# Optimization experiments

Hardware: AMD Instinct MI355X
Metric: run time of the kernel (lower is better)

Reference implementation:

```python
import jax, jax.numpy as jnp
import numpy as np

N = 100_000   # nodes
E = 800_000   # edges
G = 2048      # graphs in batch
IN, H = 74, 256
M1, M2 = 1024, 512


def setup_inputs() -> dict:
    key = jax.random.key(0)
    ks = jax.random.split(key, 16)
    h = jax.random.normal(ks[0], (N, IN), dtype=jnp.float32)
    src = jax.random.randint(ks[1], (E,), 0, N, dtype=jnp.int32)
    dst = jax.random.randint(ks[2], (E,), 0, N, dtype=jnp.int32)
    gid = jnp.sort(jax.random.randint(ks[3], (N,), 0, G, dtype=jnp.int32))
    s = lambda d: 1.0 / np.sqrt(d)
    W_in = jax.random.normal(ks[4], (IN, H), dtype=jnp.float32) * s(IN)
    b_in = jnp.zeros((H,), jnp.float32)
    W_gcr = jax.random.normal(ks[5], (10, H, H), dtype=jnp.float32) * s(H)  # 5 GCR x 2 convs
    b_gcr = jnp.zeros((10, H), jnp.float32)
    W1 = jax.random.normal(ks[6], (H, M1), dtype=jnp.float32) * s(H)
    b1 = jnp.zeros((M1,), jnp.float32)
    W2 = jax.random.normal(ks[7], (M1, M2), dtype=jnp.float32) * s(M1)
    b2 = jnp.zeros((M2,), jnp.float32)
    W3 = jax.random.normal(ks[8], (M2, 1), dtype=jnp.float32) * s(M2)
    b3 = jnp.zeros((1,), jnp.float32)
    return dict(h=h, src=src, dst=dst, gid=gid, W_in=W_in, b_in=b_in,
                W_gcr=W_gcr, b_gcr=b_gcr, W1=W1, b1=b1, W2=W2, b2=b2, W3=W3, b3=b3)


def _graph_conv(x, W, b, src, dst, out_norm, in_norm):
    # DGL GraphConv, norm='both': D_out^{-1/2} -> SpMM(copy_u,sum) -> D_in^{-1/2} -> linear
    x = x * out_norm[:, None]
    m = jax.ops.segment_sum(x[src], dst, num_segments=N)
    m = m * in_norm[:, None]
    return m @ W + b


def reference(h, src, dst, gid, W_in, b_in, W_gcr, b_gcr, W1, b1, W2, b2, W3, b3):
    ones_e = jnp.ones((E,), jnp.float32)
    out_deg = jax.ops.segment_sum(ones_e, src, num_segments=N)
    in_deg = jax.ops.segment_sum(ones_e, dst, num_segments=N)
    out_norm = jax.lax.rsqrt(jnp.maximum(out_deg, 1.0))
    in_norm = jax.lax.rsqrt(jnp.maximum(in_deg, 1.0))

    x = _graph_conv(h, W_in, b_in, src, dst, out_norm, in_norm)  # no activation here
    for i in range(5):  # GCR: gcn1 -> relu -> gcn2 -> relu
        y = _graph_conv(x, W_gcr[2 * i], b_gcr[2 * i], src, dst, out_norm, in_norm)
        y = _graph_conv(jax.nn.relu(y), W_gcr[2 * i + 1], b_gcr[2 * i + 1], src, dst, out_norm, in_norm)
        x = jax.nn.relu(y)  # res_connection=0 -> plain replace

    # dgl.mean_nodes per graph
    sums = jax.ops.segment_sum(x, gid, num_segments=G)
    cnts = jax.ops.segment_sum(jnp.ones((N,), jnp.float32), gid, num_segments=G)
    node_mean = sums / jnp.maximum(cnts, 1.0)[:, None]

    z = jax.nn.leaky_relu(node_mean @ W1 + b1)
    z = jax.nn.leaky_relu(z @ W2 + b2)
    out = (z @ W3 + b3).squeeze(-1)  # [G]
    return out
```

## Files before the change

### kernel.cpp

```cpp
#include <hip/hip_runtime.h>
#include <hip/hip_bf16.h>

#define NN 100000
#define NE 800000
#define NG 2048
#define DIN 74
#define KPAD 96
#define DH 256
#define DM1 1024
#define DM2 512

typedef __attribute__((ext_vector_type(8))) short short8;
typedef __attribute__((ext_vector_type(4))) float f32x4;

__device__ inline ushort f2bf(float f) {
  unsigned u = __float_as_uint(f);
  return (ushort)((u + 0x7fffu + ((u >> 16) & 1u)) >> 16);
}
__device__ inline float bf2f(ushort h) { return __uint_as_float(((unsigned)h) << 16); }

__device__ inline void gll16(const ushort* g, ushort* l) {
  __builtin_amdgcn_global_load_lds((const __attribute__((address_space(1))) void*)g,
                                   (__attribute__((address_space(3))) void*)l, 16, 0, 0);
}

__global__ void k_deg(const int* __restrict__ src, const int* __restrict__ dst,
                      int* __restrict__ outd, int* __restrict__ ind) {
  int e = blockIdx.x * blockDim.x + threadIdx.x;
  if (e < NE) {
    atomicAdd(&outd[src[e]], 1);
    atomicAdd(&ind[dst[e]], 1);
  }
}

__global__ void k_norm(const int* __restrict__ outd, const int* __restrict__ ind,
                       float* __restrict__ onorm, float* __restrict__ inorm) {
  int i = blockIdx.x * blockDim.x + threadIdx.x;
  if (i < NN) {
    onorm[i] = rsqrtf(fmaxf((float)outd[i], 1.f));
    inorm[i] = rsqrtf(fmaxf((float)ind[i], 1.f));
  }
}

__global__ void k_scan_block(const int* __restrict__ deg, int* __restrict__ incl,
                             int* __restrict__ bsum, int n) {
  __shared__ int s[1024];
  int t = threadIdx.x;
  int i = blockIdx.x * 1024 + t;
  int v = (i < n) ? deg[i] : 0;
  s[t] = v;
  __syncthreads();
  for (int off = 1; off < 1024; off <<= 1) {
    int x = (t >= off) ? s[t - off] : 0;
    __syncthreads();
    s[t] += x;
    __syncthreads();
  }
  if (i < n) incl[i] = s[t];
  if (t == 1023) bsum[blockIdx.x] = s[1023];
}

__global__ void k_scan_sums(int* bsum, int nb) {
  int lane = threadIdx.x & 63;
  int i0 = 2 * lane, i1 = 2 * lane + 1;
  int v0 = (i0 < nb) ? bsum[i0] : 0;
  int v1 = (i1 < nb) ? bsum[i1] : 0;
  int s = v0 + v1;
  for (int off = 1; off < 64; off <<= 1) {
    int t = __shfl_up(s, off);
    if (lane >= off) s += t;
  }
  int excl = s - (v0 + v1);
  if (i0 < nb) bsum[i0] = excl;
  if (i1 < nb) bsum[i1] = excl + v0;
}

__global__ void k_scan_add(const int* __restrict__ incl, const int* __restrict__ bsum,
                           const int* __restrict__ deg,
                           int* __restrict__ offs, int* __restrict__ cursor, int n) {
  int i = blockIdx.x * blockDim.x + threadIdx.x;
  if (i < n) {
    int v = incl[i] + bsum[i >> 10];
    offs[i + 1] = v;
    cursor[i] = v - deg[i];
    if (i == 0) offs[0] = 0;
  }
}

__global__ void k_scatter(const int* __restrict__ src, const int* __restrict__ dst,
                          int* __restrict__ cursor, int* __restrict__ ssrc) {
  int e = blockIdx.x * blockDim.x + threadIdx.x;
  if (e < NE) {
    int pos = atomicAdd(&cursor[dst[e]], 1);
    ssrc[pos] = src[e];
  }
}

__global__ void k_convw(const float* __restrict__ W_in, const float* __restrict__ W_gcr,
                        const float* __restrict__ W1, const float* __restrict__ W2,
                        ushort* __restrict__ Wt0h, ushort* __restrict__ Wt0l,
                        ushort* __restrict__ Wtgh, ushort* __restrict__ Wtgl,
                        ushort* __restrict__ Wt1h, ushort* __restrict__ Wt1l,
                        ushort* __restrict__ Wt2h, ushort* __restrict__ Wt2l) {
  int idx = blockIdx.x * blockDim.x + threadIdx.x;
  const int n0 = 256 * KPAD;
  const int n1 = n0 + 10 * 65536;
  const int n2 = n1 + DM1 * DH;
  const int n3 = n2 + DM2 * DM1;
  float v;
  ushort *dh, *dl;
  int o;
  if (idx < n0) {
    int n = idx / KPAD, k = idx - n * KPAD;
    v = (k < DIN) ? W_in[k * DH + n] : 0.f;
    dh = Wt0h; dl = Wt0l; o = idx;
  } else if (idx < n1) {
    int j = idx - n0;
    int l = j >> 16, r = j & 65535;
    int n = r >> 8, k = r & 255;
    v = W_gcr[l * 65536 + k * 256 + n];
    dh = Wtgh; dl = Wtgl; o = l * 65536 + n * 256 + k;
  } else if (idx < n2) {
    int j = idx - n1;
    int n = j >> 8, k = j & 255;
    v = W1[k * DM1 + n];
    dh = Wt1h; dl = Wt1l; o = n * 256 + k;
  } else if (idx < n3) {
    int j = idx - n2;
    int n = j >> 10, k = j & 1023;
    v = W2[k * DM2 + n];
    dh = Wt2h; dl = Wt2l; o = n * 1024 + k;
  } else {
    return;
  }
  ushort hv = f2bf(v);
  dh[o] = hv;
  dl[o] = f2bf(v - bf2f(hv));
}

__global__ void k_spmm74(const float* __restrict__ h, const int* __restrict__ offs,
                         const int* __restrict__ ssrc, const float* __restrict__ onorm,
                         const float* __restrict__ inorm,
                         ushort* __restrict__ Ahi, ushort* __restrict__ Alo) {
  int row = blockIdx.x * 4 + (threadIdx.x >> 6);
  if (row >= NN) return;
  int lane = threadIdx.x & 63;
  int beg = offs[row], end = offs[row + 1];
  float a0 = 0.f, a1 = 0.f;
  for (int e = beg; e < end; ++e) {
    int s = ssrc[e];
    float w = onorm[s];
    const float* hr = h + (size_t)s * DIN;
    a0 += w * hr[lane];
    if (lane < DIN - 64) a1 += w * hr[64 + lane];
  }
  float win = inorm[row];
  ushort* ph = Ahi + (size_t)row * KPAD;
  ushort* pl = Alo + (size_t)row * KPAD;
  float v0 = a0 * win;
  ushort h0 = f2bf(v0);
  ph[lane] = h0;
  pl[lane] = f2bf(v0 - bf2f(h0));
  if (lane < DIN - 64) {
    float v1 = a1 * win;
    ushort h1 = f2bf(v1);
    ph[64 + lane] = h1;
    pl[64 + lane] = f2bf(v1 - bf2f(h1));
  } else if (lane < KPAD - 64) {
    ph[64 + lane] = 0;
    pl[64 + lane] = 0;
  }
}

__global__ void k_spmm256(const ushort* __restrict__ xh, const int* __restrict__ offs,
                          const int* __restrict__ ssrc, const float* __restrict__ onorm,
                          const float* __restrict__ inorm,
                          ushort* __restrict__ Ahi, ushort* __restrict__ Alo) {
  int row = blockIdx.x * 4 + (threadIdx.x >> 6);
  if (row >= NN) return;
  int lane = threadIdx.x & 63;
  int beg = offs[row], n = offs[row + 1] - beg;
  float a0 = 0.f, a1 = 0.f, a2 = 0.f, a3 = 0.f;
  float w0 = 0.f, w1 = 0.f, w2 = 0.f, w3 = 0.f;
  uint2 z = {0, 0};
  uint2 u0 = z, u1 = z, u2 = z, u3 = z;
#define LOADJ(wj, uj, idx) { int s_ = ssrc[idx]; wj = onorm[s_]; \
    uj = *(const uint2*)(xh + (size_t)s_ * DH + lane * 4); }
  if (n > 0) LOADJ(w0, u0, beg)
  if (n > 1) LOADJ(w1, u1, beg + 1)
  if (n > 2) LOADJ(w2, u2, beg + 2)
  if (n > 3) LOADJ(w3, u3, beg + 3)
  int e = 0;
#define STEP(wj, uj) { float fw = wj; uint2 fu = uj; \
    if (e + 4 < n) LOADJ(wj, uj, beg + e + 4) \
    a0 += fw * __uint_as_float(fu.x << 16); \
    a1 += fw * __uint_as_float(fu.x & 0xffff0000u); \
    a2 += fw * __uint_as_float(fu.y << 16); \
    a3 += fw * __uint_as_float(fu.y & 0xffff0000u); ++e; }
  while (e < n) {
    STEP(w0, u0) if (e >= n) break;
    STEP(w1, u1) if (e >= n) break;
    STEP(w2, u2) if (e >= n) break;
    STEP(w3, u3)
  }
#undef STEP
#undef LOADJ
  float win = inorm[row];
  float o[4] = {a0 * win, a1 * win, a2 * win, a3 * win};
  ushort4 hv, lv;
  hv.x = f2bf(o[0]); lv.x = f2bf(o[0] - bf2f(hv.x));
  hv.y = f2bf(o[1]); lv.y = f2bf(o[1] - bf2f(hv.y));
  hv.z = f2bf(o[2]); lv.z = f2bf(o[2] - bf2f(hv.z));
  hv.w = f2bf(o[3]); lv.w = f2bf(o[3] - bf2f(hv.w));
  *(ushort4*)(Ahi + (size_t)row * DH + lane * 4) = hv;
  *(ushort4*)(Alo + (size_t)row * DH + lane * 4) = lv;
}

template <int ACT, int OUT>
__global__ __launch_bounds__(512, 4) void k_mfma(
    const ushort* __restrict__ Ah, const ushort* __restrict__ Al,
    const ushort* __restrict__ Bh, const ushort* __restrict__ Bl,
    const float* __restrict__ bias, void* __restrict__ C0, void* __restrict__ C1,
    int M, int K, int Nc) {
  __shared__ __align__(16) ushort Ash[128 * 32], Asl[128 * 32];
  __shared__ __align__(16) ushort Bsh[256 * 32], Bsl[256 * 32];
  const int tid = threadIdx.x, lane = tid & 63, wv = tid >> 6;
  const int wm = (wv >> 2) * 64, wn = (wv & 3) * 64;
  const int quad = lane >> 4, l15 = lane & 15;
  const int r0 = blockIdx.x * 128, c0 = blockIdx.y * 256;

  const int srow = lane >> 2, clds = lane & 3;
  const int arow = 16 * wv + srow;
  const int acg = clds ^ ((arow >> 1) & 3);
  int agr = r0 + arow; if (agr > M - 1) agr = M - 1;
  const size_t aoff = (size_t)agr * K + acg * 8;
  const int brow0 = 16 * wv + srow, brow1 = brow0 + 128;
  const int bcg0 = clds ^ ((brow0 >> 1) & 3);
  const int bcg1 = clds ^ ((brow1 >> 1) & 3);
  const size_t boff0 = (size_t)(c0 + brow0) * K + bcg0 * 8;
  const size_t boff1 = (size_t)(c0 + brow1) * K + bcg1 * 8;
  ushort* lAh = &Ash[(16 * wv) * 32];
  ushort* lAl = &Asl[(16 * wv) * 32];
  ushort* lB0h = &Bsh[(16 * wv) * 32];
  ushort* lB0l = &Bsl[(16 * wv) * 32];
  ushort* lB1h = &Bsh[(16 * wv + 128) * 32];
  ushort* lB1l = &Bsl[(16 * wv + 128) * 32];

  f32x4 acc[4][4] = {};
  const int nk = K >> 5;
  for (int s = 0; s < nk; ++s) {
    const int k0 = s << 5;
    __syncthreads();
    gll16(Ah + aoff + k0, lAh);
    gll16(Al + aoff + k0, lAl);
    gll16(Bh + boff0 + k0, lB0h);
    gll16(Bl + boff0 + k0, lB0l);
    gll16(Bh + boff1 + k0, lB1h);
    gll16(Bl + boff1 + k0, lB1l);
    __syncthreads();
    short8 ah[4], al[4];
#pragma unroll
    for (int t = 0; t < 4; ++t) {
      int r = wm + t * 16 + l15;
      int sa = (quad ^ ((r >> 1) & 3)) << 3;
      ah[t] = *(const short8*)&Ash[r * 32 + sa];
      al[t] = *(const short8*)&Asl[r * 32 + sa];
    }
#pragma unroll
    for (int nt = 0; nt < 4; ++nt) {
      int rb = wn + nt * 16 + l15;
      int sb = (quad ^ ((rb >> 1) & 3)) << 3;
      short8 bh = *(const short8*)&Bsh[rb * 32 + sb];
      short8 bl = *(const short8*)&Bsl[rb * 32 + sb];
#pragma unroll
      for (int mt = 0; mt < 4; ++mt) {
        acc[mt][nt] = __builtin_amdgcn_mfma_f32_16x16x32_bf16(ah[mt], bh, acc[mt][nt], 0, 0, 0);
        acc[mt][nt] = __builtin_amdgcn_mfma_f32_16x16x32_bf16(ah[mt], bl, acc[mt][nt], 0, 0, 0);
        acc[mt][nt] = __builtin_amdgcn_mfma_f32_16x16x32_bf16(al[mt], bh, acc[mt][nt], 0, 0, 0);
      }
    }
  }

  float bv[4];
#pragma unroll
  for (int nt = 0; nt < 4; ++nt) bv[nt] = bias[c0 + wn + nt * 16 + l15];
#pragma unroll
  for (int mt = 0; mt < 4; ++mt) {
#pragma unroll
    for (int r = 0; r < 4; ++r) {
      int gr = r0 + wm + mt * 16 + quad * 4 + r;
      if (gr >= M) continue;
#pragma unroll
      for (int nt = 0; nt < 4; ++nt) {
        int gc = c0 + wn + nt * 16 + l15;
        float v = acc[mt][nt][r] + bv[nt];
        if (ACT == 1) v = fmaxf(v, 0.f);
        if (ACT == 2) v = (v > 0.f) ? v : 0.01f * v;
        size_t idx = (size_t)gr * Nc + gc;
        if (OUT == 0) {
          ((float*)C0)[idx] = v;
        } else if (OUT == 1) {
          ((ushort*)C0)[idx] = f2bf(v);
        } else {
          ushort hv = f2bf(v);
          ((ushort*)C0)[idx] = hv;
          ((ushort*)C1)[idx] = f2bf(v - bf2f(hv));
        }
      }
    }
  }
}

__global__ void k_gbounds(const int* __restrict__ gid, int* __restrict__ gstart) {
  int g = blockIdx.x * blockDim.x + threadIdx.x;
  if (g > NG) return;
  int lo = 0, hi = NN;
  while (lo < hi) {
    int mid = (lo + hi) >> 1;
    if (gid[mid] < g) lo = mid + 1; else hi = mid;
  }
  gstart[g] = lo;
}

__global__ void k_pool(const ushort* __restrict__ xh, const int* __restrict__ gstart,
                       ushort* __restrict__ ph, ushort* __restrict__ pl) {
  int g = blockIdx.x * 4 + (threadIdx.x >> 6);
  if (g >= NG) return;
  int lane = threadIdx.x & 63;
  int beg = gstart[g], end = gstart[g + 1];
  float a0 = 0.f, a1 = 0.f, a2 = 0.f, a3 = 0.f;
  for (int r = beg; r < end; ++r) {
    uint2 u = *(const uint2*)(xh + (size_t)r * DH + lane * 4);
    a0 += __uint_as_float(u.x << 16);
    a1 += __uint_as_float(u.x & 0xffff0000u);
    a2 += __uint_as_float(u.y << 16);
    a3 += __uint_as_float(u.y & 0xffff0000u);
  }
  float inv = 1.f / fmaxf((float)(end - beg), 1.f);
  float o[4] = {a0 * inv, a1 * inv, a2 * inv, a3 * inv};
  ushort4 hv, lv;
  hv.x = f2bf(o[0]); lv.x = f2bf(o[0] - bf2f(hv.x));
  hv.y = f2bf(o[1]); lv.y = f2bf(o[1] - bf2f(hv.y));
  hv.z = f2bf(o[2]); lv.z = f2bf(o[2] - bf2f(hv.z));
  hv.w = f2bf(o[3]); lv.w = f2bf(o[3] - bf2f(hv.w));
  *(ushort4*)(ph + (size_t)g * DH + lane * 4) = hv;
  *(ushort4*)(pl + (size_t)g * DH + lane * 4) = lv;
}

__global__ void k_out(const float* __restrict__ z2, const float* __restrict__ W3,
                      const float* __restrict__ b3, float* __restrict__ out) {
  int g = blockIdx.x * 4 + (threadIdx.x >> 6);
  if (g >= NG) return;
  int lane = threadIdx.x & 63;
  float s = 0.f;
  const float* zr = z2 + (size_t)g * DM2;
  for (int k = lane; k < DM2; k += 64) s += zr[k] * W3[k];
  for (int off = 32; off > 0; off >>= 1) s += __shfl_down(s, off);
  if (lane == 0) out[g] = s + b3[0];
}

extern "C" void kernel_launch(void* const* d_in, const int* in_sizes, int n_in,
                              void* d_out, int out_size, void* d_ws, size_t ws_size,
                              hipStream_t stream) {
  (void)in_sizes; (void)n_in; (void)out_size; (void)ws_size;
  const float* h     = (const float*)d_in[0];
  const int*   src   = (const int*)d_in[1];
  const int*   dst   = (const int*)d_in[2];
  const int*   gid   = (const int*)d_in[3];
  const float* W_in  = (const float*)d_in[4];
  const float* b_in  = (const float*)d_in[5];
  const float* W_gcr = (const float*)d_in[6];
  const float* b_gcr = (const float*)d_in[7];
  const float* W1    = (const float*)d_in[8];
  const float* b1    = (const float*)d_in[9];
  const float* W2    = (const float*)d_in[10];
  const float* b2    = (const float*)d_in[11];
  const float* W3    = (const float*)d_in[12];
  const float* b3    = (const float*)d_in[13];
  float* out = (float*)d_out;

  char* p = (char*)d_ws;
  auto alloc = [&](size_t bytes) {
    char* q = p;
    p += (bytes + 255) & ~(size_t)255;
    return q;
  };
  int*    outdeg = (int*)alloc((size_t)NN * 4);
  int*    indeg  = (int*)alloc((size_t)NN * 4);
  float*  onorm  = (float*)alloc((size_t)NN * 4);
  float*  inorm  = (float*)alloc((size_t)NN * 4);
  int*    incl   = (int*)alloc((size_t)NN * 4);
  int*    bsum   = (int*)alloc(128 * 4);
  int*    offs   = (int*)alloc((size_t)(NN + 1) * 4);
  int*    cursor = (int*)alloc((size_t)NN * 4);
  int*    ssrc   = (int*)alloc((size_t)NE * 4);
  int*    gstart = (int*)alloc((size_t)(NG + 1) * 4);
  ushort* xh     = (ushort*)alloc((size_t)NN * DH * 2);
  ushort* Ahi    = (ushort*)alloc((size_t)NN * DH * 2);
  ushort* Alo    = (ushort*)alloc((size_t)NN * DH * 2);
  ushort* Wt0h   = (ushort*)alloc((size_t)256 * KPAD * 2);
  ushort* Wt0l   = (ushort*)alloc((size_t)256 * KPAD * 2);
  ushort* Wtgh   = (ushort*)alloc((size_t)10 * 65536 * 2);
  ushort* Wtgl   = (ushort*)alloc((size_t)10 * 65536 * 2);
  ushort* Wt1h   = (ushort*)alloc((size_t)DM1 * DH * 2);
  ushort* Wt1l   = (ushort*)alloc((size_t)DM1 * DH * 2);
  ushort* Wt2h   = (ushort*)alloc((size_t)DM2 * DM1 * 2);
  ushort* Wt2l   = (ushort*)alloc((size_t)DM2 * DM1 * 2);
  ushort* plh    = (ushort*)alloc((size_t)NG * DH * 2);
  ushort* pll    = (ushort*)alloc((size_t)NG * DH * 2);
  ushort* z1h    = (ushort*)alloc((size_t)NG * DM1 * 2);
  ushort* z1l    = (ushort*)alloc((size_t)NG * DM1 * 2);
  float*  z2     = (float*)alloc((size_t)NG * DM2 * 4);

  hipMemsetAsync(outdeg, 0, (size_t)NN * 4, stream);
  hipMemsetAsync(indeg, 0, (size_t)NN * 4, stream);
  k_deg<<<(NE + 255) / 256, 256, 0, stream>>>(src, dst, outdeg, indeg);
  k_norm<<<(NN + 255) / 256, 256, 0, stream>>>(outdeg, indeg, onorm, inorm);
  int nb = (NN + 1023) / 1024;
  k_scan_block<<<nb, 1024, 0, stream>>>(indeg, incl, bsum, NN);
  k_scan_sums<<<1, 64, 0, stream>>>(bsum, nb);
  k_scan_add<<<(NN + 255) / 256, 256, 0, stream>>>(incl, bsum, indeg, offs, cursor, NN);
  k_scatter<<<(NE + 255) / 256, 256, 0, stream>>>(src, dst, cursor, ssrc);

  const int nconv = 256 * KPAD + 10 * 65536 + DM1 * DH + DM2 * DM1;
  k_convw<<<(nconv + 255) / 256, 256, 0, stream>>>(W_in, W_gcr, W1, W2,
                                                   Wt0h, Wt0l, Wtgh, Wtgl,
                                                   Wt1h, Wt1l, Wt2h, Wt2l);

  dim3 gmm((NN + 127) / 128, 1);

  k_spmm74<<<(NN + 3) / 4, 256, 0, stream>>>(h, offs, ssrc, onorm, inorm, Ahi, Alo);
  k_mfma<0, 1><<<gmm, 512, 0, stream>>>(Ahi, Alo, Wt0h, Wt0l, b_in, xh, nullptr,
                                        NN, KPAD, DH);

  for (int li = 0; li < 10; ++li) {
    k_spmm256<<<(NN + 3) / 4, 256, 0, stream>>>(xh, offs, ssrc, onorm, inorm, Ahi, Alo);
    k_mfma<1, 1><<<gmm, 512, 0, stream>>>(Ahi, Alo, Wtgh + (size_t)li * 65536,
                                          Wtgl + (size_t)li * 65536, b_gcr + li * 256,
                                          xh, nullptr, NN, DH, DH);
  }

  k_gbounds<<<(NG + 1 + 255) / 256, 256, 0, stream>>>(gid, gstart);
  k_pool<<<(NG + 3) / 4, 256, 0, stream>>>(xh, gstart, plh, pll);

  dim3 gt1(NG / 128, DM1 / 256);
  k_mfma<2, 2><<<gt1, 512, 0, stream>>>(plh, pll, Wt1h, Wt1l, b1, z1h, z1l,
                                        NG, DH, DM1);
  dim3 gt2(NG / 128, DM2 / 256);
  k_mfma<2, 0><<<gt2, 512, 0, stream>>>(z1h, z1l, Wt2h, Wt2l, b2, z2, nullptr,
                                        NG, DM1, DM2);
  k_out<<<(NG + 3) / 4, 256, 0, stream>>>(z2, W3, b3, out);
}
```

Measured before the change: 1.849 ms.

## Fuse SpMM gather with MFMA GEMM per layer and prescale rows by out-norm

Replaces the separate SpMM and GEMM kernels of each GCN layer with one fused kernel. Each block of 64 rows gathers neighbour sums for two 128-column chunks straight into LDS as hi/lo bf16, then runs the MFMA against the layer weight. The out-degree norm is folded into the previous layer's epilogue, so the gather is a plain sum. The input features are also pre-converted to bf16 and pre-scaled, which lets the first SpMM read packed 48-word rows. This removes the round trip of the 256-wide aggregated matrix through global memory. In exchange, gather latency now sits inside the GEMM block, with fewer blocks and more serialisation between gathering and compute.

Result: slower. 5.401 ms (+192.0%).

```diff
diff --git a/kernel.cpp b/kernel.cpp
--- a/kernel.cpp
+++ b/kernel.cpp
@@ -138,89 +138,182 @@
   dl[o] = f2bf(v - bf2f(hv));
 }
 
-__global__ void k_spmm74(const float* __restrict__ h, const int* __restrict__ offs,
-                         const int* __restrict__ ssrc, const float* __restrict__ onorm,
-                         const float* __restrict__ inorm,
+__global__ void k_conv_h(const float* __restrict__ h, const float* __restrict__ onorm,
+                         uint* __restrict__ hb) {
+  int idx = blockIdx.x * blockDim.x + threadIdx.x;
+  if (idx >= NN * 48) return;
+  int r = idx / 48, j = idx - r * 48;
+  float s = onorm[r];
+  int k0 = j * 2;
+  float v0 = (k0 < DIN) ? h[(size_t)r * DIN + k0] * s : 0.f;
+  float v1 = (k0 + 1 < DIN) ? h[(size_t)r * DIN + k0 + 1] * s : 0.f;
+  hb[idx] = (uint)f2bf(v0) | ((uint)f2bf(v1) << 16);
+}
+
+__global__ void k_spmm74(const uint* __restrict__ hb, const int* __restrict__ offs,
+                         const int* __restrict__ ssrc, const float* __restrict__ inorm,
                          ushort* __restrict__ Ahi, ushort* __restrict__ Alo) {
   int row = blockIdx.x * 4 + (threadIdx.x >> 6);
   if (row >= NN) return;
   int lane = threadIdx.x & 63;
-  int beg = offs[row], end = offs[row + 1];
+  int beg = offs[row], n = offs[row + 1] - beg;
+  bool act = lane < 48;
+  const uint* xb = hb + lane;
   float a0 = 0.f, a1 = 0.f;
-  for (int e = beg; e < end; ++e) {
-    int s = ssrc[e];
-    float w = onorm[s];
-    const float* hr = h + (size_t)s * DIN;
-    a0 += w * hr[lane];
-    if (lane < DIN - 64) a1 += w * hr[64 + lane];
+  uint d0 = 0, d1 = 0;
+  if (n > 0 && act) d0 = xb[(size_t)ssrc[beg] * 48];
+  if (n > 1 && act) d1 = xb[(size_t)ssrc[beg + 1] * 48];
+  for (int e = 0; e < n; ++e) {
+    uint u = d0;
+    d0 = d1;
+    if (e + 2 < n && act) d1 = xb[(size_t)ssrc[beg + e + 2] * 48];
+    a0 += __uint_as_float(u << 16);
+    a1 += __uint_as_float(u & 0xffff0000u);
   }
   float win = inorm[row];
-  ushort* ph = Ahi + (size_t)row * KPAD;
-  ushort* pl = Alo + (size_t)row * KPAD;
-  float v0 = a0 * win;
-  ushort h0 = f2bf(v0);
-  ph[lane] = h0;
-  pl[lane] = f2bf(v0 - bf2f(h0));
-  if (lane < DIN - 64) {
-    float v1 = a1 * win;
-    ushort h1 = f2bf(v1);
-    ph[64 + lane] = h1;
-    pl[64 + lane] = f2bf(v1 - bf2f(h1));
-  } else if (lane < KPAD - 64) {
-    ph[64 + lane] = 0;
-    pl[64 + lane] = 0;
-  }
-}
-
-__global__ void k_spmm256(const ushort* __restrict__ xh, const int* __restrict__ offs,
-                          const int* __restrict__ ssrc, const float* __restrict__ onorm,
-                          const float* __restrict__ inorm,
-                          ushort* __restrict__ Ahi, ushort* __restrict__ Alo) {
-  int row = blockIdx.x * 4 + (threadIdx.x >> 6);
-  if (row >= NN) return;
-  int lane = threadIdx.x & 63;
-  int beg = offs[row], n = offs[row + 1] - beg;
-  float a0 = 0.f, a1 = 0.f, a2 = 0.f, a3 = 0.f;
-  float w0 = 0.f, w1 = 0.f, w2 = 0.f, w3 = 0.f;
-  uint2 z = {0, 0};
-  uint2 u0 = z, u1 = z, u2 = z, u3 = z;
-#define LOADJ(wj, uj, idx) { int s_ = ssrc[idx]; wj = onorm[s_]; \
-    uj = *(const uint2*)(xh + (size_t)s_ * DH + lane * 4); }
-  if (n > 0) LOADJ(w0, u0, beg)
-  if (n > 1) LOADJ(w1, u1, beg + 1)
-  if (n > 2) LOADJ(w2, u2, beg + 2)
-  if (n > 3) LOADJ(w3, u3, beg + 3)
-  int e = 0;
-#define STEP(wj, uj) { float fw = wj; uint2 fu = uj; \
-    if (e + 4 < n) LOADJ(wj, uj, beg + e + 4) \
-    a0 += fw * __uint_as_float(fu.x << 16); \
-    a1 += fw * __uint_as_float(fu.x & 0xffff0000u); \
-    a2 += fw * __uint_as_float(fu.y << 16); \
-    a3 += fw * __uint_as_float(fu.y & 0xffff0000u); ++e; }
-  while (e < n) {
-    STEP(w0, u0) if (e >= n) break;
-    STEP(w1, u1) if (e >= n) break;
-    STEP(w2, u2) if (e >= n) break;
-    STEP(w3, u3)
-  }
-#undef STEP
-#undef LOADJ
-  float win = inorm[row];
-  float o[4] = {a0 * win, a1 * win, a2 * win, a3 * win};
-  ushort4 hv, lv;
-  hv.x = f2bf(o[0]); lv.x = f2bf(o[0] - bf2f(hv.x));
-  hv.y = f2bf(o[1]); lv.y = f2bf(o[1] - bf2f(hv.y));
-  hv.z = f2bf(o[2]); lv.z = f2bf(o[2] - bf2f(hv.z));
-  hv.w = f2bf(o[3]); lv.w = f2bf(o[3] - bf2f(hv.w));
-  *(ushort4*)(Ahi + (size_t)row * DH + lane * 4) = hv;
-  *(ushort4*)(Alo + (size_t)row * DH + lane * 4) = lv;
-}
-
-template <int ACT, int OUT>
+  float v0 = a0 * win, v1 = a1 * win;
+  ushort h0 = f2bf(v0), h1 = f2bf(v1);
+  ushort l0 = f2bf(v0 - bf2f(h0)), l1 = f2bf(v1 - bf2f(h1));
+  if (act) {
+    *(uint*)&Ahi[(size_t)row * KPAD + lane * 2] = (uint)h0 | ((uint)h1 << 16);
+    *(uint*)&Alo[(size_t)row * KPAD + lane * 2] = (uint)l0 | ((uint)l1 << 16);
+  }
+}
+
+template <int SCALE>
+__global__ __launch_bounds__(256) void k_fused(
+    const ushort* __restrict__ xin, const int* __restrict__ offs,
+    const int* __restrict__ ssrc, const float* __restrict__ inorm,
+    const float* __restrict__ oscale,
+    const ushort* __restrict__ Bh, const ushort* __restrict__ Bl,
+    const float* __restrict__ bias, ushort* __restrict__ xout, int M) {
+  __shared__ __align__(16) ushort Ash[4 * 64 * 32], Asl[4 * 64 * 32];
+  __shared__ __align__(16) ushort Bsh[256 * 32], Bsl[256 * 32];
+  const int tid = threadIdx.x, lane = tid & 63, wv = tid >> 6;
+  const int wn = wv * 64;
+  const int quad = lane >> 4, l15 = lane & 15;
+  const int r0 = blockIdx.x * 64;
+
+  const int gsub = lane >> 4;
+  const int gc = (lane & 15) >> 2;
+  const int gpos = (lane & 3) * 2;
+  const int bsrow = lane >> 2, bclds = lane & 3;
+
+  f32x4 acc[4][4] = {};
+
+  const int rb = r0 + wv * 16;
+  int rend = rb + 16;
+  if (rend > M) rend = M;
+  const bool wvalid = (rb < M);
+  const int ebeg = wvalid ? offs[rb] : 0;
+  const int eend = wvalid ? offs[rend] : 0;
+
+  for (int kc = 0; kc < 2; ++kc) {
+    __syncthreads();
+    {
+      const ushort* xb = xin + kc * 128 + lane * 2;
+      int row = rb;
+      int rlim = wvalid ? offs[row + 1] : 0;
+      float a0 = 0.f, a1 = 0.f;
+      auto flushrow = [&](int r, float win) {
+        int tr = wv * 16 + (r - rb);
+        int addr = gsub * 2048 + tr * 32 + ((gc ^ ((tr >> 1) & 3)) << 3) + gpos;
+        float v0 = a0 * win, v1 = a1 * win;
+        ushort h0 = f2bf(v0), h1 = f2bf(v1);
+        *(uint*)&Ash[addr] = (uint)h0 | ((uint)h1 << 16);
+        ushort l0 = f2bf(v0 - bf2f(h0)), l1 = f2bf(v1 - bf2f(h1));
+        *(uint*)&Asl[addr] = (uint)l0 | ((uint)l1 << 16);
+      };
+      uint d0 = 0, d1 = 0, d2 = 0, d3 = 0;
+      int cnt = eend - ebeg;
+#define GLOADF(dj, idx) dj = *(const uint*)(xb + (size_t)ssrc[idx] * DH);
+      if (cnt > 0) GLOADF(d0, ebeg)
+      if (cnt > 1) GLOADF(d1, ebeg + 1)
+      if (cnt > 2) GLOADF(d2, ebeg + 2)
+      if (cnt > 3) GLOADF(d3, ebeg + 3)
+      int e = ebeg;
+#define GSTEPF(dj) { \
+      while (e >= rlim) { flushrow(row, inorm[row]); a0 = a1 = 0.f; ++row; rlim = offs[row + 1]; } \
+      uint u = dj; if (e + 4 < eend) GLOADF(dj, e + 4) \
+      a0 += __uint_as_float(u << 16); a1 += __uint_as_float(u & 0xffff0000u); ++e; }
+      while (e < eend) {
+        GSTEPF(d0) if (e >= eend) break;
+        GSTEPF(d1) if (e >= eend) break;
+        GSTEPF(d2) if (e >= eend) break;
+        GSTEPF(d3)
+      }
+#undef GSTEPF
+#undef GLOADF
+      while (row < rb + 16) {
+        float win = (row < M) ? inorm[row] : 0.f;
+        flushrow(row, win);
+        a0 = a1 = 0.f;
+        ++row;
+      }
+    }
+    __syncthreads();
+    for (int s = 0; s < 4; ++s) {
+      const int k0 = kc * 128 + s * 32;
+#pragma unroll
+      for (int i = 0; i < 4; ++i) {
+        int rowb = i * 64 + 16 * wv + bsrow;
+        int cg = bclds ^ ((rowb >> 1) & 3);
+        size_t go = (size_t)rowb * DH + k0 + cg * 8;
+        gll16(Bh + go, &Bsh[(i * 64 + 16 * wv) * 32]);
+        gll16(Bl + go, &Bsl[(i * 64 + 16 * wv) * 32]);
+      }
+      __syncthreads();
+      short8 ah[4], al[4];
+#pragma unroll
+      for (int t = 0; t < 4; ++t) {
+        int r = t * 16 + l15;
+        int sa = (quad ^ ((r >> 1) & 3)) << 3;
+        ah[t] = *(const short8*)&Ash[s * 2048 + r * 32 + sa];
+        al[t] = *(const short8*)&Asl[s * 2048 + r * 32 + sa];
+      }
+#pragma unroll
+      for (int nt = 0; nt < 4; ++nt) {
+        int rbq = wn + nt * 16 + l15;
+        int sb = (quad ^ ((rbq >> 1) & 3)) << 3;
+        short8 bh = *(const short8*)&Bsh[rbq * 32 + sb];
+        short8 bl = *(const short8*)&Bsl[rbq * 32 + sb];
+#pragma unroll
+        for (int mt = 0; mt < 4; ++mt) {
+          acc[mt][nt] = __builtin_amdgcn_mfma_f32_16x16x32_bf16(ah[mt], bh, acc[mt][nt], 0, 0, 0);
+          acc[mt][nt] = __builtin_amdgcn_mfma_f32_16x16x32_bf16(ah[mt], bl, acc[mt][nt], 0, 0, 0);
+          acc[mt][nt] = __builtin_amdgcn_mfma_f32_16x16x32_bf16(al[mt], bh, acc[mt][nt], 0, 0, 0);
+        }
+      }
+      __syncthreads();
+    }
+  }
+
+  float bv[4];
+#pragma unroll
+  for (int nt = 0; nt < 4; ++nt) bv[nt] = bias[wn + nt * 16 + l15];
+#pragma unroll
+  for (int mt = 0; mt < 4; ++mt) {
+#pragma unroll
+    for (int r = 0; r < 4; ++r) {
+      int gr = r0 + mt * 16 + quad * 4 + r;
+      if (gr >= M) continue;
+      float osc = SCALE ? oscale[gr] : 1.f;
+#pragma unroll
+      for (int nt = 0; nt < 4; ++nt) {
+        float v = fmaxf(acc[mt][nt][r] + bv[nt], 0.f);
+        if (SCALE) v *= osc;
+        xout[(size_t)gr * DH + wn + nt * 16 + l15] = f2bf(v);
+      }
+    }
+  }
+}
+
+template <int ACT, int OUT, int SCALE>
 __global__ __launch_bounds__(512, 4) void k_mfma(
     const ushort* __restrict__ Ah, const ushort* __restrict__ Al,
     const ushort* __restrict__ Bh, const ushort* __restrict__ Bl,
-    const float* __restrict__ bias, void* __restrict__ C0, void* __restrict__ C1,
+    const float* __restrict__ bias, const float* __restrict__ oscale,
+    void* __restrict__ C0, void* __restrict__ C1,
     int M, int K, int Nc) {
   __shared__ __align__(16) ushort Ash[128 * 32], Asl[128 * 32];
   __shared__ __align__(16) ushort Bsh[256 * 32], Bsl[256 * 32];
@@ -232,7 +325,8 @@
   const int srow = lane >> 2, clds = lane & 3;
   const int arow = 16 * wv + srow;
   const int acg = clds ^ ((arow >> 1) & 3);
-  int agr = r0 + arow; if (agr > M - 1) agr = M - 1;
+  int agr = r0 + arow;
+  if (agr > M - 1) agr = M - 1;
   const size_t aoff = (size_t)agr * K + acg * 8;
   const int brow0 = 16 * wv + srow, brow1 = brow0 + 128;
   const int bcg0 = clds ^ ((brow0 >> 1) & 3);
@@ -290,12 +384,14 @@
     for (int r = 0; r < 4; ++r) {
       int gr = r0 + wm + mt * 16 + quad * 4 + r;
       if (gr >= M) continue;
+      float osc = SCALE ? oscale[gr] : 1.f;
 #pragma unroll
       for (int nt = 0; nt < 4; ++nt) {
         int gc = c0 + wn + nt * 16 + l15;
         float v = acc[mt][nt][r] + bv[nt];
         if (ACT == 1) v = fmaxf(v, 0.f);
         if (ACT == 2) v = (v > 0.f) ? v : 0.01f * v;
+        if (SCALE) v *= osc;
         size_t idx = (size_t)gr * Nc + gc;
         if (OUT == 0) {
           ((float*)C0)[idx] = v;
@@ -395,9 +491,11 @@
   int*    cursor = (int*)alloc((size_t)NN * 4);
   int*    ssrc   = (int*)alloc((size_t)NE * 4);
   int*    gstart = (int*)alloc((size_t)(NG + 1) * 4);
-  ushort* xh     = (ushort*)alloc((size_t)NN * DH * 2);
-  ushort* Ahi    = (ushort*)alloc((size_t)NN * DH * 2);
-  ushort* Alo    = (ushort*)alloc((size_t)NN * DH * 2);
+  uint*   hb     = (uint*)alloc((size_t)NN * 48 * 4);
+  ushort* xh0    = (ushort*)alloc((size_t)NN * DH * 2);
+  ushort* xh1    = (ushort*)alloc((size_t)NN * DH * 2);
+  ushort* Ahi    = (ushort*)alloc((size_t)NN * KPAD * 2);
+  ushort* Alo    = (ushort*)alloc((size_t)NN * KPAD * 2);
   ushort* Wt0h   = (ushort*)alloc((size_t)256 * KPAD * 2);
   ushort* Wt0l   = (ushort*)alloc((size_t)256 * KPAD * 2);
   ushort* Wtgh   = (ushort*)alloc((size_t)10 * 65536 * 2);
@@ -426,28 +524,36 @@
   k_convw<<<(nconv + 255) / 256, 256, 0, stream>>>(W_in, W_gcr, W1, W2,
                                                    Wt0h, Wt0l, Wtgh, Wtgl,
                                                    Wt1h, Wt1l, Wt2h, Wt2l);
-
+  k_conv_h<<<(NN * 48 + 255) / 256, 256, 0, stream>>>(h, onorm, hb);
+
+  k_spmm74<<<(NN + 3) / 4, 256, 0, stream>>>(hb, offs, ssrc, inorm, Ahi, Alo);
   dim3 gmm((NN + 127) / 128, 1);
-
-  k_spmm74<<<(NN + 3) / 4, 256, 0, stream>>>(h, offs, ssrc, onorm, inorm, Ahi, Alo);
-  k_mfma<0, 1><<<gmm, 512, 0, stream>>>(Ahi, Alo, Wt0h, Wt0l, b_in, xh, nullptr,
-                                        NN, KPAD, DH);
-
+  k_mfma<0, 1, 1><<<gmm, 512, 0, stream>>>(Ahi, Alo, Wt0h, Wt0l, b_in, onorm,
+                                           xh0, nullptr, NN, KPAD, DH);
+
+  ushort* xin = xh0;
+  ushort* xout = xh1;
   for (int li = 0; li < 10; ++li) {
-    k_spmm256<<<(NN + 3) / 4, 256, 0, stream>>>(xh, offs, ssrc, onorm, inorm, Ahi, Alo);
-    k_mfma<1, 1><<<gmm, 512, 0, stream>>>(Ahi, Alo, Wtgh + (size_t)li * 65536,
-                                          Wtgl + (size_t)li * 65536, b_gcr + li * 256,
-                                          xh, nullptr, NN, DH, DH);
+    const ushort* bh = Wtgh + (size_t)li * 65536;
+    const ushort* bl = Wtgl + (size_t)li * 65536;
+    const float* bb = b_gcr + li * 256;
+    if (li < 9)
+      k_fused<1><<<(NN + 63) / 64, 256, 0, stream>>>(xin, offs, ssrc, inorm, onorm,
+                                                     bh, bl, bb, xout, NN);
+    else
+      k_fused<0><<<(NN + 63) / 64, 256, 0, stream>>>(xin, offs, ssrc, inorm, onorm,
+                                                     bh, bl, bb, xout, NN);
+    ushort* t = xin; xin = xout; xout = t;
   }
 
   k_gbounds<<<(NG + 1 + 255) / 256, 256, 0, stream>>>(gid, gstart);
-  k_pool<<<(NG + 3) / 4, 256, 0, stream>>>(xh, gstart, plh, pll);
+  k_pool<<<(NG + 3) / 4, 256, 0, stream>>>(xin, gstart, plh, pll);
 
   dim3 gt1(NG / 128, DM1 / 256);
-  k_mfma<2, 2><<<gt1, 512, 0, stream>>>(plh, pll, Wt1h, Wt1l, b1, z1h, z1l,
-                                        NG, DH, DM1);
+  k_mfma<2, 2, 0><<<gt1, 512, 0, stream>>>(plh, pll, Wt1h, Wt1l, b1, nullptr,
+                                           z1h, z1l, NG, DH, DM1);
   dim3 gt2(NG / 128, DM2 / 256);
-  k_mfma<2, 0><<<gt2, 512, 0, stream>>>(z1h, z1l, Wt2h, Wt2l, b2, z2, nullptr,
-                                        NG, DM1, DM2);
+  k_mfma<2, 0, 0><<<gt2, 512, 0, stream>>>(z1h, z1l, Wt2h, Wt2l, b2, nullptr,
+                                           z2, nullptr, NG, DM1, DM2);
   k_out<<<(NG + 3) / 4, 256, 0, stream>>>(z2, W3, b3, out);
 }
```

## Fold out-degree norm into GEMM epilogue and drop low-part activation MFMA

Applied to the files above, without the earlier changes.

Moves the source out-degree scaling from the SpMM gather into the GEMM epilogue, so the stored features are already prescaled and the gather no longer loads onorm per edge. Precomputes the 74-wide input features as packed, prescaled bf16 and gathers them 2 per lane. Drops the bf16 low-part activation buffer and its MFMA term for the 256-wide layers, which cuts SpMM writes, GEMM A-loads and one third of the MFMAs. It also ping-pongs the activation buffers. The cost is lower accuracy, since activations now carry only bf16 precision instead of the split hi/lo representation.

Result: faster. 1.698 ms (-8.2%).

```diff
diff --git a/kernel.cpp b/kernel.cpp
--- a/kernel.cpp
+++ b/kernel.cpp
@@ -138,91 +138,97 @@
   dl[o] = f2bf(v - bf2f(hv));
 }
 
-__global__ void k_spmm74(const float* __restrict__ h, const int* __restrict__ offs,
-                         const int* __restrict__ ssrc, const float* __restrict__ onorm,
-                         const float* __restrict__ inorm,
+__global__ void k_conv_h(const float* __restrict__ h, const float* __restrict__ onorm,
+                         uint* __restrict__ hb) {
+  int idx = blockIdx.x * blockDim.x + threadIdx.x;
+  if (idx >= NN * 48) return;
+  int r = idx / 48, j = idx - r * 48;
+  float s = onorm[r];
+  int k0 = j * 2;
+  float v0 = (k0 < DIN) ? h[(size_t)r * DIN + k0] * s : 0.f;
+  float v1 = (k0 + 1 < DIN) ? h[(size_t)r * DIN + k0 + 1] * s : 0.f;
+  hb[idx] = (uint)f2bf(v0) | ((uint)f2bf(v1) << 16);
+}
+
+__global__ void k_spmm74(const uint* __restrict__ hb, const int* __restrict__ offs,
+                         const int* __restrict__ ssrc, const float* __restrict__ inorm,
                          ushort* __restrict__ Ahi, ushort* __restrict__ Alo) {
   int row = blockIdx.x * 4 + (threadIdx.x >> 6);
   if (row >= NN) return;
   int lane = threadIdx.x & 63;
-  int beg = offs[row], end = offs[row + 1];
+  int beg = offs[row], n = offs[row + 1] - beg;
+  bool act = lane < 48;
+  const uint* xb = hb + lane;
   float a0 = 0.f, a1 = 0.f;
-  for (int e = beg; e < end; ++e) {
-    int s = ssrc[e];
-    float w = onorm[s];
-    const float* hr = h + (size_t)s * DIN;
-    a0 += w * hr[lane];
-    if (lane < DIN - 64) a1 += w * hr[64 + lane];
+  uint d0 = 0, d1 = 0;
+  if (n > 0 && act) d0 = xb[(size_t)ssrc[beg] * 48];
+  if (n > 1 && act) d1 = xb[(size_t)ssrc[beg + 1] * 48];
+  for (int e = 0; e < n; ++e) {
+    uint u = d0;
+    d0 = d1;
+    if (e + 2 < n && act) d1 = xb[(size_t)ssrc[beg + e + 2] * 48];
+    a0 += __uint_as_float(u << 16);
+    a1 += __uint_as_float(u & 0xffff0000u);
   }
   float win = inorm[row];
-  ushort* ph = Ahi + (size_t)row * KPAD;
-  ushort* pl = Alo + (size_t)row * KPAD;
-  float v0 = a0 * win;
-  ushort h0 = f2bf(v0);
-  ph[lane] = h0;
-  pl[lane] = f2bf(v0 - bf2f(h0));
-  if (lane < DIN - 64) {
-    float v1 = a1 * win;
-    ushort h1 = f2bf(v1);
-    ph[64 + lane] = h1;
-    pl[64 + lane] = f2bf(v1 - bf2f(h1));
-  } else if (lane < KPAD - 64) {
-    ph[64 + lane] = 0;
-    pl[64 + lane] = 0;
-  }
-}
-
-__global__ void k_spmm256(const ushort* __restrict__ xh, const int* __restrict__ offs,
-                          const int* __restrict__ ssrc, const float* __restrict__ onorm,
-                          const float* __restrict__ inorm,
-                          ushort* __restrict__ Ahi, ushort* __restrict__ Alo) {
+  float v0 = a0 * win, v1 = a1 * win;
+  ushort h0 = f2bf(v0), h1 = f2bf(v1);
+  ushort l0 = f2bf(v0 - bf2f(h0)), l1 = f2bf(v1 - bf2f(h1));
+  if (act) {
+    *(uint*)&Ahi[(size_t)row * KPAD + lane * 2] = (uint)h0 | ((uint)h1 << 16);
+    *(uint*)&Alo[(size_t)row * KPAD + lane * 2] = (uint)l0 | ((uint)l1 << 16);
+  }
+}
+
+__global__ void k_spmm1(const ushort* __restrict__ xin, const int* __restrict__ offs,
+                        const int* __restrict__ ssrc, const float* __restrict__ inorm,
+                        ushort* __restrict__ Ah) {
   int row = blockIdx.x * 4 + (threadIdx.x >> 6);
   if (row >= NN) return;
   int lane = threadIdx.x & 63;
   int beg = offs[row], n = offs[row + 1] - beg;
   float a0 = 0.f, a1 = 0.f, a2 = 0.f, a3 = 0.f;
-  float w0 = 0.f, w1 = 0.f, w2 = 0.f, w3 = 0.f;
   uint2 z = {0, 0};
   uint2 u0 = z, u1 = z, u2 = z, u3 = z;
-#define LOADJ(wj, uj, idx) { int s_ = ssrc[idx]; wj = onorm[s_]; \
-    uj = *(const uint2*)(xh + (size_t)s_ * DH + lane * 4); }
-  if (n > 0) LOADJ(w0, u0, beg)
-  if (n > 1) LOADJ(w1, u1, beg + 1)
-  if (n > 2) LOADJ(w2, u2, beg + 2)
-  if (n > 3) LOADJ(w3, u3, beg + 3)
+#define LOADJ(uj, idx) { int s_ = ssrc[idx]; \
+    uj = *(const uint2*)(xin + (size_t)s_ * DH + lane * 4); }
+  if (n > 0) LOADJ(u0, beg)
+  if (n > 1) LOADJ(u1, beg + 1)
+  if (n > 2) LOADJ(u2, beg + 2)
+  if (n > 3) LOADJ(u3, beg + 3)
   int e = 0;
-#define STEP(wj, uj) { float fw = wj; uint2 fu = uj; \
-    if (e + 4 < n) LOADJ(wj, uj, beg + e + 4) \
-    a0 += fw * __uint_as_float(fu.x << 16); \
-    a1 += fw * __uint_as_float(fu.x & 0xffff0000u); \
-    a2 += fw * __uint_as_float(fu.y << 16); \
-    a3 += fw * __uint_as_float(fu.y & 0xffff0000u); ++e; }
+#define STEP(uj) { uint2 fu = uj; \
+    if (e + 4 < n) LOADJ(uj, beg + e + 4) \
+    a0 += __uint_as_float(fu.x << 16); \
+    a1 += __uint_as_float(fu.x & 0xffff0000u); \
+    a2 += __uint_as_float(fu.y << 16); \
+    a3 += __uint_as_float(fu.y & 0xffff0000u); ++e; }
   while (e < n) {
-    STEP(w0, u0) if (e >= n) break;
-    STEP(w1, u1) if (e >= n) break;
-    STEP(w2, u2) if (e >= n) break;
-    STEP(w3, u3)
+    STEP(u0) if (e >= n) break;
+    STEP(u1) if (e >= n) break;
+    STEP(u2) if (e >= n) break;
+    STEP(u3)
   }
 #undef STEP
 #undef LOADJ
   float win = inorm[row];
-  float o[4] = {a0 * win, a1 * win, a2 * win, a3 * win};
-  ushort4 hv, lv;
-  hv.x = f2bf(o[0]); lv.x = f2bf(o[0] - bf2f(hv.x));
-  hv.y = f2bf(o[1]); lv.y = f2bf(o[1] - bf2f(hv.y));
-  hv.z = f2bf(o[2]); lv.z = f2bf(o[2] - bf2f(hv.z));
-  hv.w = f2bf(o[3]); lv.w = f2bf(o[3] - bf2f(hv.w));
-  *(ushort4*)(Ahi + (size_t)row * DH + lane * 4) = hv;
-  *(ushort4*)(Alo + (size_t)row * DH + lane * 4) = lv;
-}
-
-template <int ACT, int OUT>
+  ushort4 hv;
+  hv.x = f2bf(a0 * win);
+  hv.y = f2bf(a1 * win);
+  hv.z = f2bf(a2 * win);
+  hv.w = f2bf(a3 * win);
+  *(ushort4*)(Ah + (size_t)row * DH + lane * 4) = hv;
+}
+
+template <int ACT, int OUT, int SCALE, int ALO>
 __global__ __launch_bounds__(512, 4) void k_mfma(
     const ushort* __restrict__ Ah, const ushort* __restrict__ Al,
     const ushort* __restrict__ Bh, const ushort* __restrict__ Bl,
-    const float* __restrict__ bias, void* __restrict__ C0, void* __restrict__ C1,
+    const float* __restrict__ bias, const float* __restrict__ oscale,
+    void* __restrict__ C0, void* __restrict__ C1,
     int M, int K, int Nc) {
-  __shared__ __align__(16) ushort Ash[128 * 32], Asl[128 * 32];
+  __shared__ __align__(16) ushort Ash[128 * 32];
+  __shared__ __align__(16) ushort Asl[ALO ? 128 * 32 : 8];
   __shared__ __align__(16) ushort Bsh[256 * 32], Bsl[256 * 32];
   const int tid = threadIdx.x, lane = tid & 63, wv = tid >> 6;
   const int wm = (wv >> 2) * 64, wn = (wv & 3) * 64;
@@ -232,7 +238,8 @@
   const int srow = lane >> 2, clds = lane & 3;
   const int arow = 16 * wv + srow;
   const int acg = clds ^ ((arow >> 1) & 3);
-  int agr = r0 + arow; if (agr > M - 1) agr = M - 1;
+  int agr = r0 + arow;
+  if (agr > M - 1) agr = M - 1;
   const size_t aoff = (size_t)agr * K + acg * 8;
   const int brow0 = 16 * wv + srow, brow1 = brow0 + 128;
   const int bcg0 = clds ^ ((brow0 >> 1) & 3);
@@ -240,7 +247,7 @@
   const size_t boff0 = (size_t)(c0 + brow0) * K + bcg0 * 8;
   const size_t boff1 = (size_t)(c0 + brow1) * K + bcg1 * 8;
   ushort* lAh = &Ash[(16 * wv) * 32];
-  ushort* lAl = &Asl[(16 * wv) * 32];
+  ushort* lAl = &Asl[ALO ? (16 * wv) * 32 : 0];
   ushort* lB0h = &Bsh[(16 * wv) * 32];
   ushort* lB0l = &Bsl[(16 * wv) * 32];
   ushort* lB1h = &Bsh[(16 * wv + 128) * 32];
@@ -252,7 +259,7 @@
     const int k0 = s << 5;
     __syncthreads();
     gll16(Ah + aoff + k0, lAh);
-    gll16(Al + aoff + k0, lAl);
+    if (ALO) gll16(Al + aoff + k0, lAl);
     gll16(Bh + boff0 + k0, lB0h);
     gll16(Bl + boff0 + k0, lB0l);
     gll16(Bh + boff1 + k0, lB1h);
@@ -264,7 +271,7 @@
       int r = wm + t * 16 + l15;
       int sa = (quad ^ ((r >> 1) & 3)) << 3;
       ah[t] = *(const short8*)&Ash[r * 32 + sa];
-      al[t] = *(const short8*)&Asl[r * 32 + sa];
+      if (ALO) al[t] = *(const short8*)&Asl[r * 32 + sa];
     }
 #pragma unroll
     for (int nt = 0; nt < 4; ++nt) {
@@ -276,7 +283,8 @@
       for (int mt = 0; mt < 4; ++mt) {
         acc[mt][nt] = __builtin_amdgcn_mfma_f32_16x16x32_bf16(ah[mt], bh, acc[mt][nt], 0, 0, 0);
         acc[mt][nt] = __builtin_amdgcn_mfma_f32_16x16x32_bf16(ah[mt], bl, acc[mt][nt], 0, 0, 0);
-        acc[mt][nt] = __builtin_amdgcn_mfma_f32_16x16x32_bf16(al[mt], bh, acc[mt][nt], 0, 0, 0);
+        if (ALO)
+          acc[mt][nt] = __builtin_amdgcn_mfma_f32_16x16x32_bf16(al[mt], bh, acc[mt][nt], 0, 0, 0);
       }
     }
   }
@@ -290,12 +298,14 @@
     for (int r = 0; r < 4; ++r) {
       int gr = r0 + wm + mt * 16 + quad * 4 + r;
       if (gr >= M) continue;
+      float osc = SCALE ? oscale[gr] : 1.f;
 #pragma unroll
       for (int nt = 0; nt < 4; ++nt) {
         int gc = c0 + wn + nt * 16 + l15;
         float v = acc[mt][nt][r] + bv[nt];
         if (ACT == 1) v = fmaxf(v, 0.f);
         if (ACT == 2) v = (v > 0.f) ? v : 0.01f * v;
+        if (SCALE) v *= osc;
         size_t idx = (size_t)gr * Nc + gc;
         if (OUT == 0) {
           ((float*)C0)[idx] = v;
@@ -395,9 +405,12 @@
   int*    cursor = (int*)alloc((size_t)NN * 4);
   int*    ssrc   = (int*)alloc((size_t)NE * 4);
   int*    gstart = (int*)alloc((size_t)(NG + 1) * 4);
-  ushort* xh     = (ushort*)alloc((size_t)NN * DH * 2);
-  ushort* Ahi    = (ushort*)alloc((size_t)NN * DH * 2);
-  ushort* Alo    = (ushort*)alloc((size_t)NN * DH * 2);
+  uint*   hb     = (uint*)alloc((size_t)NN * 48 * 4);
+  ushort* xh0    = (ushort*)alloc((size_t)NN * DH * 2);
+  ushort* xh1    = (ushort*)alloc((size_t)NN * DH * 2);
+  ushort* Ah1    = (ushort*)alloc((size_t)NN * DH * 2);
+  ushort* A0h    = (ushort*)alloc((size_t)NN * KPAD * 2);
+  ushort* A0l    = (ushort*)alloc((size_t)NN * KPAD * 2);
   ushort* Wt0h   = (ushort*)alloc((size_t)256 * KPAD * 2);
   ushort* Wt0l   = (ushort*)alloc((size_t)256 * KPAD * 2);
   ushort* Wtgh   = (ushort*)alloc((size_t)10 * 65536 * 2);
@@ -426,28 +439,37 @@
   k_convw<<<(nconv + 255) / 256, 256, 0, stream>>>(W_in, W_gcr, W1, W2,
                                                    Wt0h, Wt0l, Wtgh, Wtgl,
                                                    Wt1h, Wt1l, Wt2h, Wt2l);
-
+  k_conv_h<<<(NN * 48 + 255) / 256, 256, 0, stream>>>(h, onorm, hb);
+
+  k_spmm74<<<(NN + 3) / 4, 256, 0, stream>>>(hb, offs, ssrc, inorm, A0h, A0l);
   dim3 gmm((NN + 127) / 128, 1);
-
-  k_spmm74<<<(NN + 3) / 4, 256, 0, stream>>>(h, offs, ssrc, onorm, inorm, Ahi, Alo);
-  k_mfma<0, 1><<<gmm, 512, 0, stream>>>(Ahi, Alo, Wt0h, Wt0l, b_in, xh, nullptr,
-                                        NN, KPAD, DH);
-
+  k_mfma<0, 1, 1, 1><<<gmm, 512, 0, stream>>>(A0h, A0l, Wt0h, Wt0l, b_in, onorm,
+                                              xh0, nullptr, NN, KPAD, DH);
+
+  ushort* xin = xh0;
+  ushort* xout = xh1;
   for (int li = 0; li < 10; ++li) {
-    k_spmm256<<<(NN + 3) / 4, 256, 0, stream>>>(xh, offs, ssrc, onorm, inorm, Ahi, Alo);
-    k_mfma<1, 1><<<gmm, 512, 0, stream>>>(Ahi, Alo, Wtgh + (size_t)li * 65536,
-                                          Wtgl + (size_t)li * 65536, b_gcr + li * 256,
-                                          xh, nullptr, NN, DH, DH);
+    k_spmm1<<<(NN + 3) / 4, 256, 0, stream>>>(xin, offs, ssrc, inorm, Ah1);
+    const ushort* bh = Wtgh + (size_t)li * 65536;
+    const ushort* bl = Wtgl + (size_t)li * 65536;
+    const float* bb = b_gcr + li * 256;
+    if (li < 9)
+      k_mfma<1, 1, 1, 0><<<gmm, 512, 0, stream>>>(Ah1, nullptr, bh, bl, bb, onorm,
+                                                  xout, nullptr, NN, DH, DH);
+    else
+      k_mfma<1, 1, 0, 0><<<gmm, 512, 0, stream>>>(Ah1, nullptr, bh, bl, bb, nullptr,
+                                                  xout, nullptr, NN, DH, DH);
+    ushort* t = xin; xin = xout; xout = t;
   }
 
   k_gbounds<<<(NG + 1 + 255) / 256, 256, 0, stream>>>(gid, gstart);
-  k_pool<<<(NG + 3) / 4, 256, 0, stream>>>(xh, gstart, plh, pll);
+  k_pool<<<(NG + 3) / 4, 256, 0, stream>>>(xin, gstart, plh, pll);
 
   dim3 gt1(NG / 128, DM1 / 256);
-  k_mfma<2, 2><<<gt1, 512, 0, stream>>>(plh, pll, Wt1h, Wt1l, b1, z1h, z1l,
-                                        NG, DH, DM1);
+  k_mfma<2, 2, 0, 1><<<gt1, 512, 0, stream>>>(plh, pll, Wt1h, Wt1l, b1, nullptr,
+                                              z1h, z1l, NG, DH, DM1);
   dim3 gt2(NG / 128, DM2 / 256);
-  k_mfma<2, 0><<<gt2, 512, 0, stream>>>(z1h, z1l, Wt2h, Wt2l, b2, z2, nullptr,
-                                        NG, DM1, DM2);
+  k_mfma<2, 0, 0, 1><<<gt2, 512, 0, stream>>>(z1h, z1l, Wt2h, Wt2l, b2, nullptr,
+                                              z2, nullptr, NG, DM1, DM2);
   k_out<<<(NG + 3) / 4, 256, 0, stream>>>(z2, W3, b3, out);
 }
```
